# Kernel optimization log

Measured on AMD Instinct MI355X. Metric: run time of the kernel, lower is better.

## Reference

```python
import jax, jax.numpy as jnp
import numpy as np

N_NODES = 50000
N_EDGES = 800000
IN_DIM = 256
HID = [256, 128]
NEG_SLOPE = 0.01  # F.leaky_relu default


def setup_inputs() -> dict:
    key = jax.random.key(0)
    ks = jax.random.split(key, 8)
    x = jax.random.normal(ks[0], (N_NODES, IN_DIM), dtype=jnp.float32)
    w1 = jax.random.normal(ks[1], (IN_DIM, HID[0]), dtype=jnp.float32) * (1.0 / np.sqrt(IN_DIM))
    b1 = jnp.zeros((HID[0],), dtype=jnp.float32)
    w2 = jax.random.normal(ks[2], (HID[0], HID[1]), dtype=jnp.float32) * (1.0 / np.sqrt(HID[0]))
    b2 = jnp.zeros((HID[1],), dtype=jnp.float32)
    src = jax.random.randint(ks[3], (N_EDGES,), 0, N_NODES, dtype=jnp.int32)
    dst = jax.random.randint(ks[4], (N_EDGES,), 0, N_NODES, dtype=jnp.int32)
    edge_weight = jax.random.uniform(ks[5], (N_EDGES,), dtype=jnp.float32)
    return {"x": x, "w1": w1, "b1": b1, "w2": w2, "b2": b2,
            "src": src, "dst": dst, "edge_weight": edge_weight}


def _gcn_layer(h, w, b, src, dst, ew, n_nodes):
    # GraphConvolution: support = h @ W ; out = spmm(adj, support) + b
    support = h @ w                              # [N, d_out]
    msg = support[src] * ew[:, None]             # [E, d_out] gather + scale
    agg = jax.ops.segment_sum(msg, dst, num_segments=n_nodes)  # [N, d_out]
    return agg + b


def reference(x, w1, b1, w2, b2, src, dst, edge_weight):
    # layer 1: GCN -> leaky_relu -> dropout(eval: identity)
    h = _gcn_layer(x, w1, b1, src, dst, edge_weight, N_NODES)
    h = jax.nn.leaky_relu(h, NEG_SLOPE)
    # layer 2
    h = _gcn_layer(h, w2, b2, src, dst, edge_weight, N_NODES)
    h = jax.nn.leaky_relu(h, NEG_SLOPE)
    return h
```

## Files before the change

### kernel.cpp

```cpp
#include <hip/hip_runtime.h>

#define NEG_SLOPE 0.01f

constexpr int N_NODES_C = 50000;
constexpr int N_EDGES_C = 800000;
constexpr int M_PAD = 50048;
constexpr int META_CAP = 950016;

typedef short bf16x8 __attribute__((ext_vector_type(8)));
typedef float f32x4 __attribute__((ext_vector_type(4)));

__device__ inline unsigned short f2bf(float f) {
  unsigned int u = __float_as_uint(f);
  u += 0x7FFF + ((u >> 16) & 1);
  return (unsigned short)(u >> 16);
}
__device__ inline float bf2f(unsigned int h16) {
  return __uint_as_float(h16 << 16);
}

constexpr int NB_CONVX = (M_PAD * 8) / 256;
constexpr int NB_W1 = (256 * 256) / 256;
constexpr int NB_W2 = (256 * 128) / 256;
constexpr int NB_HIST = ((N_EDGES_C / 4) + 255) / 256;
constexpr int NB_NONH = NB_CONVX + NB_W1 + NB_W2;
constexpr int NB_PRE = NB_NONH + NB_HIST;
constexpr int NB_IL = 2 * NB_HIST;

__global__ __launch_bounds__(256) void pre_kernel(
    const float* __restrict__ x, const float* __restrict__ w1,
    const float* __restrict__ w2, const int* __restrict__ dst,
    unsigned short* __restrict__ xb, unsigned short* __restrict__ w1T,
    unsigned short* __restrict__ w2T, int* __restrict__ counts) {
  const int bx = blockIdx.x;
  const int tid = threadIdx.x;
  int l = 0, isHist = 0, h = 0;
  if (bx < NB_IL) {
    if (bx & 1) { isHist = 1; h = bx >> 1; }
    else l = bx >> 1;
  } else {
    l = bx - NB_HIST;
  }

  if (isHist) {
    int e = (h * 256 + tid) * 4;
    if (e < N_EDGES_C) {
      int4 d4 = *(const int4*)(dst + e);
      atomicAdd(&counts[d4.x], 1);
      atomicAdd(&counts[d4.y], 1);
      atomicAdd(&counts[d4.z], 1);
      atomicAdd(&counts[d4.w], 1);
    }
  } else if (l < NB_CONVX) {
    int idx = l * 256 + tid;
    int row = idx >> 3;
    int c32 = (idx & 7) * 32;
    uint4 o[4];
    if (row < N_NODES_C) {
      const float4* p = (const float4*)(x + (size_t)row * 256 + c32);
      float4 f[8];
#pragma unroll
      for (int i = 0; i < 8; ++i) f[i] = p[i];
#pragma unroll
      for (int i = 0; i < 4; ++i) {
        o[i].x = f2bf(f[2 * i].x) | ((unsigned)f2bf(f[2 * i].y) << 16);
        o[i].y = f2bf(f[2 * i].z) | ((unsigned)f2bf(f[2 * i].w) << 16);
        o[i].z = f2bf(f[2 * i + 1].x) | ((unsigned)f2bf(f[2 * i + 1].y) << 16);
        o[i].w = f2bf(f[2 * i + 1].z) | ((unsigned)f2bf(f[2 * i + 1].w) << 16);
      }
    } else {
#pragma unroll
      for (int i = 0; i < 4; ++i) o[i] = make_uint4(0, 0, 0, 0);
    }
#pragma unroll
    for (int i = 0; i < 4; ++i)
      *(uint4*)(xb + (size_t)row * 256 + c32 + i * 8) = o[i];
  } else if (l < NB_CONVX + NB_W1) {
    int idx = (l - NB_CONVX) * 256 + tid;
    int n = idx >> 8, k = idx & 255;
    w1T[idx] = f2bf(w1[(size_t)k * 256 + n]);
  } else {
    int idx = (l - NB_CONVX - NB_W1) * 256 + tid;
    int n = idx >> 8, k = idx & 255;
    w2T[idx] = f2bf(w2[(size_t)k * 128 + n]);
  }
}

constexpr int NB_NODE = (N_NODES_C + 255) / 256;
constexpr int NB_SCAT = (M_PAD + 255) / 256;

__global__ __launch_bounds__(256) void hist_kernel(const int* __restrict__ counts,
                                                   int* __restrict__ hist2,
                                                   int* __restrict__ ehist) {
  __shared__ int lh[64], le[64];
  const int t = threadIdx.x;
  if (t < 64) { lh[t] = 0; le[t] = 0; }
  __syncthreads();
  const int i = blockIdx.x * 256 + t;
  if (i < N_NODES_C) {
    int d = counts[i];
    int bin = d < 63 ? d : 63;
    atomicAdd(&lh[bin], 1);
    atomicAdd(&le[bin], (d + 3) & ~3);
  }
  __syncthreads();
  if (t < 64) {
    if (lh[t]) atomicAdd(&hist2[t], lh[t]);
    if (le[t]) atomicAdd(&ehist[t], le[t]);
  }
}

__global__ __launch_bounds__(256) void scatter_kernel(
    const int* __restrict__ counts, const int* __restrict__ hist2,
    const int* __restrict__ ehist, int* __restrict__ gclaim_n,
    int* __restrict__ gclaim_e, int* __restrict__ perm,
    int* __restrict__ nstart, int* __restrict__ ndeg,
    int* __restrict__ cursor, unsigned* __restrict__ s_meta) {
  __shared__ int nbase[64], ebase[64], lh[64], le[64], gn[64], ge[64];
  const int t = threadIdx.x;
  if (t < 64) {
    int hv = hist2[t], ev = ehist[t];
    int xs = hv, xe = ev;
#pragma unroll
    for (int off = 1; off < 64; off <<= 1) {
      int a = __shfl_up(xs, off);
      int b = __shfl_up(xe, off);
      if (t >= off) { xs += a; xe += b; }
    }
    nbase[t] = xs - hv;
    ebase[t] = xe - ev;
    lh[t] = 0;
    le[t] = 0;
  }
  __syncthreads();
  const int idx = blockIdx.x * 256 + t;
  int d = -1, bin = 0, lrank = 0, erank = 0;
  if (idx < N_NODES_C) {
    d = counts[idx];
    bin = d < 63 ? d : 63;
    lrank = atomicAdd(&lh[bin], 1);
    erank = atomicAdd(&le[bin], (d + 3) & ~3);
  } else if (idx < M_PAD) {
    perm[idx] = idx;
    nstart[idx] = 0;
    ndeg[idx] = 0;
  }
  __syncthreads();
  if (t < 64) {
    gn[t] = lh[t] ? nbase[t] + atomicAdd(&gclaim_n[t], lh[t]) : 0;
    ge[t] = le[t] ? ebase[t] + atomicAdd(&gclaim_e[t], le[t]) : 0;
  }
  __syncthreads();
  if (d >= 0) {
    const int grank = gn[bin] + lrank;
    const int estart = ge[bin] + erank;
    perm[grank] = idx;
    nstart[grank] = estart;
    ndeg[grank] = d;
    cursor[idx] = estart;
    const int d4 = (d + 3) & ~3;
    for (int j = d; j < d4; ++j) s_meta[estart + j] = 0;
  }
}


#define GLOAD_LDS16(g, l)                                              \
  __builtin_amdgcn_global_load_lds(                                    \
      (__attribute__((address_space(1))) void*)(g),                    \
      (__attribute__((address_space(3))) void*)(l), 16, 0, 0)

__device__ __forceinline__ void gemm_tile(
    const unsigned short* __restrict__ A,
    const unsigned short* __restrict__ BT,
    unsigned short* __restrict__ C,
    int N, int ldc, int row0, int col0, short* Asm, short* Bsm) {
  constexpr int K = 256;
  const int tid = threadIdx.x;
  const int lane = tid & 63, wave = tid >> 6;
  const int wm = wave & 1, wn = wave >> 1;

  const int ch0 = wave * 2, ch1 = wave * 2 + 1;
  const int o0 = ch0 * 512 + lane * 8;
  const int o1 = ch1 * 512 + lane * 8;
  const int r0 = o0 >> 5, c0 = o0 & 31;
  const int r1 = o1 >> 5, c1 = o1 & 31;

  f32x4 acc[4][4] = {};

  for (int k0 = 0; k0 < K; k0 += 32) {
    GLOAD_LDS16(A + (size_t)(row0 + r0) * K + k0 + c0, &Asm[ch0 * 512]);
    GLOAD_LDS16(A + (size_t)(row0 + r1) * K + k0 + c1, &Asm[ch1 * 512]);
    GLOAD_LDS16(BT + (size_t)(col0 + r0) * K + k0 + c0, &Bsm[ch0 * 512]);
    GLOAD_LDS16(BT + (size_t)(col0 + r1) * K + k0 + c1, &Bsm[ch1 * 512]);
    __builtin_amdgcn_s_waitcnt(0);
    __syncthreads();

    bf16x8 af[4], bf[4];
#pragma unroll
    for (int mt = 0; mt < 4; ++mt)
      af[mt] = *(const bf16x8*)&Asm[(wm * 64 + mt * 16 + (lane & 15)) * 32 + (lane >> 4) * 8];
#pragma unroll
    for (int nt = 0; nt < 4; ++nt)
      bf[nt] = *(const bf16x8*)&Bsm[(wn * 64 + nt * 16 + (lane & 15)) * 32 + (lane >> 4) * 8];
#pragma unroll
    for (int mt = 0; mt < 4; ++mt)
#pragma unroll
      for (int nt = 0; nt < 4; ++nt)
        acc[mt][nt] = __builtin_amdgcn_mfma_f32_16x16x32_bf16(af[mt], bf[nt], acc[mt][nt], 0, 0, 0);
    __syncthreads();
  }

  const int cl = lane & 15, rq = (lane >> 4) * 4;
#pragma unroll
  for (int mt = 0; mt < 4; ++mt) {
    const int rbase = row0 + wm * 64 + mt * 16 + rq;
#pragma unroll
    for (int nt = 0; nt < 4; ++nt) {
      const int col = col0 + wn * 64 + nt * 16 + cl;
#pragma unroll
      for (int i = 0; i < 4; ++i)
        C[(size_t)(rbase + i) * ldc + col] = f2bf(acc[mt][nt][i]);
    }
  }
}

constexpr int NB_GEMM1 = 2 * (M_PAD / 128);
constexpr int NB_FILL = ((N_EDGES_C / 4) + 255) / 256;

__global__ __launch_bounds__(256) void fill_gemm1_kernel(
    const unsigned short* __restrict__ A, const unsigned short* __restrict__ BT,
    unsigned short* __restrict__ C, const int* __restrict__ src,
    const int* __restrict__ dst, const float* __restrict__ ew,
    int* __restrict__ cursor, unsigned* __restrict__ s_meta) {
  __shared__ short Asm[128 * 32];
  __shared__ short Bsm[128 * 32];
  const int b = blockIdx.x;
  if ((b & 1) == 0) {
    const int t = b >> 1;
    gemm_tile(A, BT, C, 256, 256, (t >> 1) * 128, (t & 1) * 128, Asm, Bsm);
  } else {
    const int g = (b >> 1) * 256 + threadIdx.x;
    const int e = g * 4;
    if (e < N_EDGES_C) {
      int4 d4 = *(const int4*)(dst + e);
      int4 s4 = *(const int4*)(src + e);
      float4 w4 = *(const float4*)(ew + e);
      unsigned m0 = (unsigned)s4.x | ((unsigned)f2bf(w4.x) << 16);
      unsigned m1 = (unsigned)s4.y | ((unsigned)f2bf(w4.y) << 16);
      unsigned m2 = (unsigned)s4.z | ((unsigned)f2bf(w4.z) << 16);
      unsigned m3 = (unsigned)s4.w | ((unsigned)f2bf(w4.w) << 16);
      int p0 = atomicAdd(&cursor[d4.x], 1);
      int p1 = atomicAdd(&cursor[d4.y], 1);
      int p2 = atomicAdd(&cursor[d4.z], 1);
      int p3 = atomicAdd(&cursor[d4.w], 1);
      __builtin_nontemporal_store(m0, s_meta + p0);
      __builtin_nontemporal_store(m1, s_meta + p1);
      __builtin_nontemporal_store(m2, s_meta + p2);
      __builtin_nontemporal_store(m3, s_meta + p3);
    }
  }
}

__global__ __launch_bounds__(256) void gemm2_kernel(
    const unsigned short* __restrict__ A, const unsigned short* __restrict__ BT,
    unsigned short* __restrict__ C) {
  __shared__ short Asm[128 * 32];
  __shared__ short Bsm[128 * 32];
  gemm_tile(A, BT, C, 128, 128, blockIdx.x * 128, 0, Asm, Bsm);
}


__device__ __forceinline__ void rfma_256(float* acc, unsigned m,
                                         const unsigned short* __restrict__ tp) {
  uint2 v = *(const uint2*)(tp + (size_t)(m & 0xffffu) * 256);
  float wt = bf2f(m >> 16);
  acc[0] += bf2f(v.x & 0xffffu) * wt;
  acc[1] += bf2f(v.x >> 16) * wt;
  acc[2] += bf2f(v.y & 0xffffu) * wt;
  acc[3] += bf2f(v.y >> 16) * wt;
}

__device__ __forceinline__ void rfma_128(float* acc, unsigned m,
                                         const unsigned short* __restrict__ tp) {
  unsigned v = *(const unsigned*)(tp + (size_t)(m & 0xffffu) * 128);
  float wt = bf2f(m >> 16);
  acc[0] += bf2f(v & 0xffffu) * wt;
  acc[1] += bf2f(v >> 16) * wt;
}

template <int OUT_D, bool OUT_BF16>
__global__ __launch_bounds__(256) void agg_row_kernel(
    const unsigned short* __restrict__ sup,
    const unsigned* __restrict__ s_meta,
    const int* __restrict__ nstart, const int* __restrict__ ndeg,
    const int* __restrict__ perm, const float* __restrict__ bias,
    unsigned short* __restrict__ out_bf, float* __restrict__ out_f, int n_total) {
  constexpr int DPL = OUT_D / 64;
  const int tid = threadIdx.x;
  const int wv = tid >> 6;
  const int lane = tid & 63;
  const int idx = blockIdx.x * 4 + wv;
  if (idx >= n_total) return;
  const int n = perm[idx];
  const bool valid = n < N_NODES_C;
  const unsigned short* tp = sup + lane * DPL;

  float acc[DPL] = {};
  const int s = nstart[idx];
  const int nq = (ndeg[idx] + 3) >> 2;
  const uint4* mp = (const uint4*)(s_meta + s);

#define RFMA(mm)                              \
  do {                                        \
    if (OUT_D == 256) rfma_256(acc, mm, tp);  \
    else rfma_128(acc, mm, tp);               \
  } while (0)

  if (nq > 0) {
    uint4 m0 = mp[0];
    uint4 m1 = (nq > 1) ? mp[1] : make_uint4(0, 0, 0, 0);
    int q = 0;
    for (; q + 2 < nq; q += 2) {
      uint4 p0 = mp[q + 2];
      uint4 p1 = mp[q + 3];
      RFMA(m0.x); RFMA(m0.y); RFMA(m0.z); RFMA(m0.w);
      RFMA(m1.x); RFMA(m1.y); RFMA(m1.z); RFMA(m1.w);
      m0 = p0;
      m1 = p1;
    }
    RFMA(m0.x); RFMA(m0.y); RFMA(m0.z); RFMA(m0.w);
    if (q + 1 < nq) { RFMA(m1.x); RFMA(m1.y); RFMA(m1.z); RFMA(m1.w); }
  }
#undef RFMA

  const int dbase = lane * DPL;
  if (OUT_BF16) {
    unsigned short o[DPL];
#pragma unroll
    for (int j = 0; j < DPL; ++j) {
      if (valid) {
        float v = acc[j] + bias[dbase + j];
        v = v >= 0.f ? v : NEG_SLOPE * v;
        o[j] = f2bf(v);
      } else {
        o[j] = 0;
      }
    }
    uint2 pk;
    pk.x = o[0] | ((unsigned)o[1] << 16);
    pk.y = o[2] | ((unsigned)o[3] << 16);
    *(uint2*)(out_bf + (size_t)n * OUT_D + dbase) = pk;
  } else if (valid) {
    float r[DPL];
#pragma unroll
    for (int j = 0; j < DPL; ++j) {
      float v = acc[j] + bias[dbase + j];
      r[j] = v >= 0.f ? v : NEG_SLOPE * v;
    }
    *(float2*)(out_f + (size_t)n * OUT_D + dbase) = make_float2(r[0], r[1]);
  }
}


extern "C" void kernel_launch(void* const* d_in, const int* in_sizes, int n_in,
                              void* d_out, int out_size, void* d_ws, size_t ws_size,
                              hipStream_t stream) {
  const float* x  = (const float*)d_in[0];
  const float* w1 = (const float*)d_in[1];
  const float* b1 = (const float*)d_in[2];
  const float* w2 = (const float*)d_in[3];
  const float* b2 = (const float*)d_in[4];
  const int*   src = (const int*)d_in[5];
  const int*   dst = (const int*)d_in[6];
  const float* ew  = (const float*)d_in[7];
  float* out = (float*)d_out;

  unsigned short* xb   = (unsigned short*)d_ws;
  unsigned short* a2b  = xb + (size_t)M_PAD * 256;
  unsigned short* sup1 = a2b + (size_t)M_PAD * 256;
  unsigned short* sup2 = sup1 + (size_t)M_PAD * 256;
  unsigned short* w1T  = sup2 + (size_t)M_PAD * 128;
  unsigned short* w2T  = w1T + 256 * 256;
  int* counts  = (int*)(w2T + 128 * 256);
  int* cursor  = counts + N_NODES_C;
  int* perm    = cursor + N_NODES_C;
  int* nstart  = perm + M_PAD;
  int* ndeg    = nstart + M_PAD;
  int* hist2   = ndeg + M_PAD;
  int* ehist   = hist2 + 64;
  int* gclaim_n= ehist + 64;
  int* gclaim_e= gclaim_n + 64;
  unsigned* s_meta = (unsigned*)(gclaim_e + 64);

  hipMemsetAsync(counts, 0, N_NODES_C * sizeof(int), stream);
  hipMemsetAsync(hist2, 0, 256 * sizeof(int), stream);
  pre_kernel<<<NB_PRE, 256, 0, stream>>>(x, w1, w2, dst, xb, w1T, w2T, counts);

  hist_kernel<<<NB_NODE, 256, 0, stream>>>(counts, hist2, ehist);
  scatter_kernel<<<NB_SCAT, 256, 0, stream>>>(counts, hist2, ehist, gclaim_n,
                                              gclaim_e, perm, nstart, ndeg,
                                              cursor, s_meta);

  fill_gemm1_kernel<<<NB_GEMM1 + NB_FILL, 256, 0, stream>>>(
      xb, w1T, sup1, src, dst, ew, cursor, s_meta);

  agg_row_kernel<256, true><<<M_PAD / 4, 256, 0, stream>>>(
      sup1, s_meta, nstart, ndeg, perm, b1, a2b, nullptr, M_PAD);

  gemm2_kernel<<<M_PAD / 128, 256, 0, stream>>>(a2b, w2T, sup2);
  agg_row_kernel<128, false><<<N_NODES_C / 4, 256, 0, stream>>>(
      sup2, s_meta, nstart, ndeg, perm, b2, nullptr, out, N_NODES_C);
}
```

Before: 296.1 us.

## Split wave across edges with 16-byte gathers and shuffle reduction in aggregation

The row-aggregation kernel now gives each lane 8 features loaded as one 16-byte vector. Sub-groups of the wave handle different edges at the same time, and a cross-lane shuffle reduction combines them at the end. This replaces narrow 4- or 8-byte gathers per lane. Separately, the x-to-bf16 conversion in pre_kernel now uses fully coalesced float4 reads, zeroes the padded rows in a dedicated block, and changes how conversion blocks are interleaved with histogram blocks. The cost is extra shuffles and idle lanes during the epilogue. The 128-dim path also reads padded metadata slots in its tail.

```diff
diff --git a/kernel.cpp b/kernel.cpp
--- a/kernel.cpp
+++ b/kernel.cpp
@@ -19,13 +19,14 @@
   return __uint_as_float(h16 << 16);
 }
 
-constexpr int NB_CONVX = (M_PAD * 8) / 256;
+constexpr int NB_CONV4 = (N_NODES_C * 64) / 1024;
+constexpr int NB_Z = 1;
 constexpr int NB_W1 = (256 * 256) / 256;
 constexpr int NB_W2 = (256 * 128) / 256;
 constexpr int NB_HIST = ((N_EDGES_C / 4) + 255) / 256;
-constexpr int NB_NONH = NB_CONVX + NB_W1 + NB_W2;
+constexpr int NB_NONH = NB_CONV4 + NB_Z + NB_W1 + NB_W2;
 constexpr int NB_PRE = NB_NONH + NB_HIST;
-constexpr int NB_IL = 2 * NB_HIST;
+constexpr int HIST_REGION = NB_HIST * 4;
 
 __global__ __launch_bounds__(256) void pre_kernel(
     const float* __restrict__ x, const float* __restrict__ w1,
@@ -34,10 +35,10 @@
     unsigned short* __restrict__ w2T, int* __restrict__ counts) {
   const int bx = blockIdx.x;
   const int tid = threadIdx.x;
-  int l = 0, isHist = 0, h = 0;
-  if (bx < NB_IL) {
-    if (bx & 1) { isHist = 1; h = bx >> 1; }
-    else l = bx >> 1;
+  int l, isHist = 0, h = 0;
+  if (bx < HIST_REGION) {
+    if ((bx & 3) == 3) { isHist = 1; h = bx >> 2; l = 0; }
+    else l = bx - ((bx + 1) >> 2);
   } else {
     l = bx - NB_HIST;
   }
@@ -51,36 +52,29 @@
       atomicAdd(&counts[d4.z], 1);
       atomicAdd(&counts[d4.w], 1);
     }
-  } else if (l < NB_CONVX) {
-    int idx = l * 256 + tid;
-    int row = idx >> 3;
-    int c32 = (idx & 7) * 32;
-    uint4 o[4];
-    if (row < N_NODES_C) {
-      const float4* p = (const float4*)(x + (size_t)row * 256 + c32);
-      float4 f[8];
-#pragma unroll
-      for (int i = 0; i < 8; ++i) f[i] = p[i];
-#pragma unroll
-      for (int i = 0; i < 4; ++i) {
-        o[i].x = f2bf(f[2 * i].x) | ((unsigned)f2bf(f[2 * i].y) << 16);
-        o[i].y = f2bf(f[2 * i].z) | ((unsigned)f2bf(f[2 * i].w) << 16);
-        o[i].z = f2bf(f[2 * i + 1].x) | ((unsigned)f2bf(f[2 * i + 1].y) << 16);
-        o[i].w = f2bf(f[2 * i + 1].z) | ((unsigned)f2bf(f[2 * i + 1].w) << 16);
-      }
-    } else {
-#pragma unroll
-      for (int i = 0; i < 4; ++i) o[i] = make_uint4(0, 0, 0, 0);
-    }
-#pragma unroll
-    for (int i = 0; i < 4; ++i)
-      *(uint4*)(xb + (size_t)row * 256 + c32 + i * 8) = o[i];
-  } else if (l < NB_CONVX + NB_W1) {
-    int idx = (l - NB_CONVX) * 256 + tid;
+  } else if (l < NB_CONV4) {
+    const float4* xv = (const float4*)x;
+#pragma unroll
+    for (int i = 0; i < 4; ++i) {
+      int g = l * 1024 + i * 256 + tid;
+      float4 f = xv[g];
+      uint2 o;
+      o.x = f2bf(f.x) | ((unsigned)f2bf(f.y) << 16);
+      o.y = f2bf(f.z) | ((unsigned)f2bf(f.w) << 16);
+      *(uint2*)(xb + (size_t)g * 4) = o;
+    }
+  } else if (l == NB_CONV4) {
+    unsigned short* base = xb + (size_t)N_NODES_C * 256;
+    uint4 z = make_uint4(0, 0, 0, 0);
+#pragma unroll
+    for (int i = 0; i < 6; ++i)
+      *(uint4*)(base + (size_t)(i * 256 + tid) * 8) = z;
+  } else if (l < NB_CONV4 + NB_Z + NB_W1) {
+    int idx = (l - NB_CONV4 - NB_Z) * 256 + tid;
     int n = idx >> 8, k = idx & 255;
     w1T[idx] = f2bf(w1[(size_t)k * 256 + n]);
   } else {
-    int idx = (l - NB_CONVX - NB_W1) * 256 + tid;
+    int idx = (l - NB_CONV4 - NB_Z - NB_W1) * 256 + tid;
     int n = idx >> 8, k = idx & 255;
     w2T[idx] = f2bf(w2[(size_t)k * 128 + n]);
   }
@@ -270,22 +264,15 @@
 }
 
 
-__device__ __forceinline__ void rfma_256(float* acc, unsigned m,
-                                         const unsigned short* __restrict__ tp) {
-  uint2 v = *(const uint2*)(tp + (size_t)(m & 0xffffu) * 256);
-  float wt = bf2f(m >> 16);
+__device__ __forceinline__ void fma8v(float* acc, uint4 v, float wt) {
   acc[0] += bf2f(v.x & 0xffffu) * wt;
   acc[1] += bf2f(v.x >> 16) * wt;
   acc[2] += bf2f(v.y & 0xffffu) * wt;
   acc[3] += bf2f(v.y >> 16) * wt;
-}
-
-__device__ __forceinline__ void rfma_128(float* acc, unsigned m,
-                                         const unsigned short* __restrict__ tp) {
-  unsigned v = *(const unsigned*)(tp + (size_t)(m & 0xffffu) * 128);
-  float wt = bf2f(m >> 16);
-  acc[0] += bf2f(v & 0xffffu) * wt;
-  acc[1] += bf2f(v >> 16) * wt;
+  acc[4] += bf2f(v.z & 0xffffu) * wt;
+  acc[5] += bf2f(v.z >> 16) * wt;
+  acc[6] += bf2f(v.w & 0xffffu) * wt;
+  acc[7] += bf2f(v.w >> 16) * wt;
 }
 
 template <int OUT_D, bool OUT_BF16>
@@ -295,7 +282,6 @@
     const int* __restrict__ nstart, const int* __restrict__ ndeg,
     const int* __restrict__ perm, const float* __restrict__ bias,
     unsigned short* __restrict__ out_bf, float* __restrict__ out_f, int n_total) {
-  constexpr int DPL = OUT_D / 64;
   const int tid = threadIdx.x;
   const int wv = tid >> 6;
   const int lane = tid & 63;
@@ -303,61 +289,92 @@
   if (idx >= n_total) return;
   const int n = perm[idx];
   const bool valid = n < N_NODES_C;
-  const unsigned short* tp = sup + lane * DPL;
-
-  float acc[DPL] = {};
   const int s = nstart[idx];
-  const int nq = (ndeg[idx] + 3) >> 2;
-  const uint4* mp = (const uint4*)(s_meta + s);
-
-#define RFMA(mm)                              \
-  do {                                        \
-    if (OUT_D == 256) rfma_256(acc, mm, tp);  \
-    else rfma_128(acc, mm, tp);               \
-  } while (0)
-
-  if (nq > 0) {
-    uint4 m0 = mp[0];
-    uint4 m1 = (nq > 1) ? mp[1] : make_uint4(0, 0, 0, 0);
-    int q = 0;
-    for (; q + 2 < nq; q += 2) {
-      uint4 p0 = mp[q + 2];
-      uint4 p1 = mp[q + 3];
-      RFMA(m0.x); RFMA(m0.y); RFMA(m0.z); RFMA(m0.w);
-      RFMA(m1.x); RFMA(m1.y); RFMA(m1.z); RFMA(m1.w);
-      m0 = p0;
-      m1 = p1;
-    }
-    RFMA(m0.x); RFMA(m0.y); RFMA(m0.z); RFMA(m0.w);
-    if (q + 1 < nq) { RFMA(m1.x); RFMA(m1.y); RFMA(m1.z); RFMA(m1.w); }
-  }
-#undef RFMA
-
-  const int dbase = lane * DPL;
-  if (OUT_BF16) {
-    unsigned short o[DPL];
-#pragma unroll
-    for (int j = 0; j < DPL; ++j) {
+  const int ne4 = ((ndeg[idx] + 3) >> 2) << 2;
+
+  float acc[8] = {};
+
+  if (OUT_D == 256) {
+    const int sub = lane >> 5;
+    const int dl = lane & 31;
+    const unsigned short* tp = sup + dl * 8;
+    for (int j = 0; j < ne4; j += 4) {
+      unsigned ma = s_meta[s + j + sub];
+      unsigned mb = s_meta[s + j + 2 + sub];
+      uint4 va = *(const uint4*)(tp + (size_t)(ma & 0xffffu) * 256);
+      uint4 vb = *(const uint4*)(tp + (size_t)(mb & 0xffffu) * 256);
+      fma8v(acc, va, bf2f(ma >> 16));
+      fma8v(acc, vb, bf2f(mb >> 16));
+    }
+#pragma unroll
+    for (int k = 0; k < 8; ++k) acc[k] += __shfl_xor(acc[k], 32);
+    if (sub == 0) {
+      const int dbase = dl * 8;
+      if (OUT_BF16) {
+        unsigned short o[8];
+#pragma unroll
+        for (int k = 0; k < 8; ++k) {
+          if (valid) {
+            float v = acc[k] + bias[dbase + k];
+            v = v >= 0.f ? v : NEG_SLOPE * v;
+            o[k] = f2bf(v);
+          } else {
+            o[k] = 0;
+          }
+        }
+        uint4 pk;
+        pk.x = o[0] | ((unsigned)o[1] << 16);
+        pk.y = o[2] | ((unsigned)o[3] << 16);
+        pk.z = o[4] | ((unsigned)o[5] << 16);
+        pk.w = o[6] | ((unsigned)o[7] << 16);
+        *(uint4*)(out_bf + (size_t)n * OUT_D + dbase) = pk;
+      } else if (valid) {
+        float r[8];
+#pragma unroll
+        for (int k = 0; k < 8; ++k) {
+          float v = acc[k] + bias[dbase + k];
+          r[k] = v >= 0.f ? v : NEG_SLOPE * v;
+        }
+        *(float4*)(out_f + (size_t)n * OUT_D + dbase) = make_float4(r[0], r[1], r[2], r[3]);
+        *(float4*)(out_f + (size_t)n * OUT_D + dbase + 4) = make_float4(r[4], r[5], r[6], r[7]);
+      }
+    }
+  } else {
+    const int sub = lane >> 4;
+    const int dl = lane & 15;
+    const unsigned short* tp = sup + dl * 8;
+    int j = 0;
+    for (; j + 8 <= ne4; j += 8) {
+      unsigned ma = s_meta[s + j + sub];
+      unsigned mb = s_meta[s + j + 4 + sub];
+      uint4 va = *(const uint4*)(tp + (size_t)(ma & 0xffffu) * 128);
+      uint4 vb = *(const uint4*)(tp + (size_t)(mb & 0xffffu) * 128);
+      fma8v(acc, va, bf2f(ma >> 16));
+      fma8v(acc, vb, bf2f(mb >> 16));
+    }
+    if (j < ne4) {
+      unsigned ma = s_meta[s + j + sub];
+      uint4 va = *(const uint4*)(tp + (size_t)(ma & 0xffffu) * 128);
+      fma8v(acc, va, bf2f(ma >> 16));
+    }
+#pragma unroll
+    for (int k = 0; k < 8; ++k) {
+      acc[k] += __shfl_xor(acc[k], 16);
+      acc[k] += __shfl_xor(acc[k], 32);
+    }
+    if (sub == 0 && lane < 16) {
+      const int dbase = dl * 8;
       if (valid) {
-        float v = acc[j] + bias[dbase + j];
-        v = v >= 0.f ? v : NEG_SLOPE * v;
-        o[j] = f2bf(v);
-      } else {
-        o[j] = 0;
+        float r[8];
+#pragma unroll
+        for (int k = 0; k < 8; ++k) {
+          float v = acc[k] + bias[dbase + k];
+          r[k] = v >= 0.f ? v : NEG_SLOPE * v;
+        }
+        *(float4*)(out_f + (size_t)n * OUT_D + dbase) = make_float4(r[0], r[1], r[2], r[3]);
+        *(float4*)(out_f + (size_t)n * OUT_D + dbase + 4) = make_float4(r[4], r[5], r[6], r[7]);
       }
     }
-    uint2 pk;
-    pk.x = o[0] | ((unsigned)o[1] << 16);
-    pk.y = o[2] | ((unsigned)o[3] << 16);
-    *(uint2*)(out_bf + (size_t)n * OUT_D + dbase) = pk;
-  } else if (valid) {
-    float r[DPL];
-#pragma unroll
-    for (int j = 0; j < DPL; ++j) {
-      float v = acc[j] + bias[dbase + j];
-      r[j] = v >= 0.f ? v : NEG_SLOPE * v;
-    }
-    *(float2*)(out_f + (size_t)n * OUT_D + dbase) = make_float2(r[0], r[1]);
   }
 }
 
```

Measured after the change: 306.1 us. 1.03x slower.

## Make degree-bucket scatter deterministic via per-block prefix counts; reshape x conversion

Applied to the files above, without the earlier changes.

The scatter kernel no longer claims bucket slots with global atomics. The histogram kernel now records per-block bucket counts, and each scatter block sums its predecessors' counts and ranks nodes with wave ballots, which gives stable, node-ordered placement and better locality. The pre-kernel's x-to-bf16 conversion is rewritten to use coalesced float4 loads with a 3:1 interleave against the histogram blocks and a separate zero-pad block. Nontemporal stores of edge metadata become plain stores. The serial per-block prefix loops (up to ~196 iterations) and the 64-iteration ballot loop add latency to the scatter kernel.

```diff
diff --git a/kernel.cpp b/kernel.cpp
--- a/kernel.cpp
+++ b/kernel.cpp
@@ -19,13 +19,14 @@
   return __uint_as_float(h16 << 16);
 }
 
-constexpr int NB_CONVX = (M_PAD * 8) / 256;
+constexpr int NB_CONV4 = (N_NODES_C * 64) / 1024;
+constexpr int NB_Z = 1;
 constexpr int NB_W1 = (256 * 256) / 256;
 constexpr int NB_W2 = (256 * 128) / 256;
 constexpr int NB_HIST = ((N_EDGES_C / 4) + 255) / 256;
-constexpr int NB_NONH = NB_CONVX + NB_W1 + NB_W2;
+constexpr int NB_NONH = NB_CONV4 + NB_Z + NB_W1 + NB_W2;
 constexpr int NB_PRE = NB_NONH + NB_HIST;
-constexpr int NB_IL = 2 * NB_HIST;
+constexpr int HIST_REGION = NB_HIST * 4;
 
 __global__ __launch_bounds__(256) void pre_kernel(
     const float* __restrict__ x, const float* __restrict__ w1,
@@ -34,10 +35,10 @@
     unsigned short* __restrict__ w2T, int* __restrict__ counts) {
   const int bx = blockIdx.x;
   const int tid = threadIdx.x;
-  int l = 0, isHist = 0, h = 0;
-  if (bx < NB_IL) {
-    if (bx & 1) { isHist = 1; h = bx >> 1; }
-    else l = bx >> 1;
+  int l, isHist = 0, h = 0;
+  if (bx < HIST_REGION) {
+    if ((bx & 3) == 3) { isHist = 1; h = bx >> 2; l = 0; }
+    else l = bx - ((bx + 1) >> 2);
   } else {
     l = bx - NB_HIST;
   }
@@ -51,36 +52,29 @@
       atomicAdd(&counts[d4.z], 1);
       atomicAdd(&counts[d4.w], 1);
     }
-  } else if (l < NB_CONVX) {
-    int idx = l * 256 + tid;
-    int row = idx >> 3;
-    int c32 = (idx & 7) * 32;
-    uint4 o[4];
-    if (row < N_NODES_C) {
-      const float4* p = (const float4*)(x + (size_t)row * 256 + c32);
-      float4 f[8];
-#pragma unroll
-      for (int i = 0; i < 8; ++i) f[i] = p[i];
-#pragma unroll
-      for (int i = 0; i < 4; ++i) {
-        o[i].x = f2bf(f[2 * i].x) | ((unsigned)f2bf(f[2 * i].y) << 16);
-        o[i].y = f2bf(f[2 * i].z) | ((unsigned)f2bf(f[2 * i].w) << 16);
-        o[i].z = f2bf(f[2 * i + 1].x) | ((unsigned)f2bf(f[2 * i + 1].y) << 16);
-        o[i].w = f2bf(f[2 * i + 1].z) | ((unsigned)f2bf(f[2 * i + 1].w) << 16);
-      }
-    } else {
-#pragma unroll
-      for (int i = 0; i < 4; ++i) o[i] = make_uint4(0, 0, 0, 0);
-    }
-#pragma unroll
-    for (int i = 0; i < 4; ++i)
-      *(uint4*)(xb + (size_t)row * 256 + c32 + i * 8) = o[i];
-  } else if (l < NB_CONVX + NB_W1) {
-    int idx = (l - NB_CONVX) * 256 + tid;
+  } else if (l < NB_CONV4) {
+    const float4* xv = (const float4*)x;
+#pragma unroll
+    for (int i = 0; i < 4; ++i) {
+      int g = l * 1024 + i * 256 + tid;
+      float4 f = xv[g];
+      uint2 o;
+      o.x = f2bf(f.x) | ((unsigned)f2bf(f.y) << 16);
+      o.y = f2bf(f.z) | ((unsigned)f2bf(f.w) << 16);
+      *(uint2*)(xb + (size_t)g * 4) = o;
+    }
+  } else if (l == NB_CONV4) {
+    unsigned short* base = xb + (size_t)N_NODES_C * 256;
+    uint4 z = make_uint4(0, 0, 0, 0);
+#pragma unroll
+    for (int i = 0; i < 6; ++i)
+      *(uint4*)(base + (size_t)(i * 256 + tid) * 8) = z;
+  } else if (l < NB_CONV4 + NB_Z + NB_W1) {
+    int idx = (l - NB_CONV4 - NB_Z) * 256 + tid;
     int n = idx >> 8, k = idx & 255;
     w1T[idx] = f2bf(w1[(size_t)k * 256 + n]);
   } else {
-    int idx = (l - NB_CONVX - NB_W1) * 256 + tid;
+    int idx = (l - NB_CONV4 - NB_Z - NB_W1) * 256 + tid;
     int n = idx >> 8, k = idx & 255;
     w2T[idx] = f2bf(w2[(size_t)k * 128 + n]);
   }
@@ -91,7 +85,9 @@
 
 __global__ __launch_bounds__(256) void hist_kernel(const int* __restrict__ counts,
                                                    int* __restrict__ hist2,
-                                                   int* __restrict__ ehist) {
+                                                   int* __restrict__ ehist,
+                                                   int* __restrict__ blk_cnt,
+                                                   int* __restrict__ blk_e63) {
   __shared__ int lh[64], le[64];
   const int t = threadIdx.x;
   if (t < 64) { lh[t] = 0; le[t] = 0; }
@@ -107,17 +103,22 @@
   if (t < 64) {
     if (lh[t]) atomicAdd(&hist2[t], lh[t]);
     if (le[t]) atomicAdd(&ehist[t], le[t]);
+    blk_cnt[blockIdx.x * 64 + t] = lh[t];
+    if (t == 63) blk_e63[blockIdx.x] = le[63];
   }
 }
 
 __global__ __launch_bounds__(256) void scatter_kernel(
     const int* __restrict__ counts, const int* __restrict__ hist2,
-    const int* __restrict__ ehist, int* __restrict__ gclaim_n,
-    int* __restrict__ gclaim_e, int* __restrict__ perm,
+    const int* __restrict__ ehist, const int* __restrict__ blk_cnt,
+    const int* __restrict__ blk_e63, int* __restrict__ perm,
     int* __restrict__ nstart, int* __restrict__ ndeg,
     int* __restrict__ cursor, unsigned* __restrict__ s_meta) {
-  __shared__ int nbase[64], ebase[64], lh[64], le[64], gn[64], ge[64];
+  __shared__ int nbase[64], ebase[64], boffn[64], wcnt[4][64], we63s[4];
+  __shared__ int boffe63;
   const int t = threadIdx.x;
+  const int wv = t >> 6, lane = t & 63;
+
   if (t < 64) {
     int hv = hist2[t], ev = ehist[t];
     int xs = hv, xe = ev;
@@ -125,40 +126,68 @@
     for (int off = 1; off < 64; off <<= 1) {
       int a = __shfl_up(xs, off);
       int b = __shfl_up(xe, off);
-      if (t >= off) { xs += a; xe += b; }
+      if (lane >= off) { xs += a; xe += b; }
     }
     nbase[t] = xs - hv;
     ebase[t] = xe - ev;
-    lh[t] = 0;
-    le[t] = 0;
-  }
-  __syncthreads();
+    int bn = 0;
+    for (int b = 0; b < (int)blockIdx.x; ++b) bn += blk_cnt[b * 64 + t];
+    boffn[t] = bn;
+  }
+  if (t == 64) {
+    int be = 0;
+    for (int b = 0; b < (int)blockIdx.x; ++b) be += blk_e63[b];
+    boffe63 = be;
+  }
+
   const int idx = blockIdx.x * 256 + t;
-  int d = -1, bin = 0, lrank = 0, erank = 0;
+  int d = -1, bin = 0, d4 = 0;
   if (idx < N_NODES_C) {
     d = counts[idx];
     bin = d < 63 ? d : 63;
-    lrank = atomicAdd(&lh[bin], 1);
-    erank = atomicAdd(&le[bin], (d + 3) & ~3);
+    d4 = (d + 3) & ~3;
   } else if (idx < M_PAD) {
     perm[idx] = idx;
     nstart[idx] = 0;
     ndeg[idx] = 0;
   }
+
+  int rank_w = 0, mycnt = 0;
+  for (int B = 0; B < 64; ++B) {
+    unsigned long long m = __ballot(d >= 0 && bin == B);
+    if (d >= 0 && bin == B)
+      rank_w = __popcll(m & ((1ull << lane) - 1));
+    if (lane == B) mycnt = __popcll(m);
+  }
+  int c63 = (d >= 0 && bin == 63) ? d4 : 0;
+  int sc = c63;
+#pragma unroll
+  for (int off = 1; off < 64; off <<= 1) {
+    int u = __shfl_up(sc, off);
+    if (lane >= off) sc += u;
+  }
+  const int excl63 = sc - c63;
+  const int tot63 = __shfl(sc, 63);
+  wcnt[wv][lane] = mycnt;
+  if (lane == 0) we63s[wv] = tot63;
   __syncthreads();
-  if (t < 64) {
-    gn[t] = lh[t] ? nbase[t] + atomicAdd(&gclaim_n[t], lh[t]) : 0;
-    ge[t] = le[t] ? ebase[t] + atomicAdd(&gclaim_e[t], le[t]) : 0;
-  }
-  __syncthreads();
+
   if (d >= 0) {
-    const int grank = gn[bin] + lrank;
-    const int estart = ge[bin] + erank;
+    int rank_blk = rank_w;
+    int e63off = excl63;
+    for (int w = 0; w < wv; ++w) {
+      rank_blk += wcnt[w][bin];
+      e63off += we63s[w];
+    }
+    const int grank = nbase[bin] + boffn[bin] + rank_blk;
+    const int d4b = (bin + 3) & ~3;
+    const int estart = (bin < 63)
+        ? ebase[bin] + (boffn[bin] + rank_blk) * d4b
+        : ebase[63] + boffe63 + e63off;
     perm[grank] = idx;
     nstart[grank] = estart;
     ndeg[grank] = d;
     cursor[idx] = estart;
-    const int d4 = (d + 3) & ~3;
     for (int j = d; j < d4; ++j) s_meta[estart + j] = 0;
   }
 }
@@ -253,10 +282,10 @@
       int p1 = atomicAdd(&cursor[d4.y], 1);
       int p2 = atomicAdd(&cursor[d4.z], 1);
       int p3 = atomicAdd(&cursor[d4.w], 1);
-      __builtin_nontemporal_store(m0, s_meta + p0);
-      __builtin_nontemporal_store(m1, s_meta + p1);
-      __builtin_nontemporal_store(m2, s_meta + p2);
-      __builtin_nontemporal_store(m3, s_meta + p3);
+      s_meta[p0] = m0;
+      s_meta[p1] = m1;
+      s_meta[p2] = m2;
+      s_meta[p3] = m3;
     }
   }
 }
@@ -388,17 +417,18 @@
   int* ndeg    = nstart + M_PAD;
   int* hist2   = ndeg + M_PAD;
   int* ehist   = hist2 + 64;
-  int* gclaim_n= ehist + 64;
-  int* gclaim_e= gclaim_n + 64;
-  unsigned* s_meta = (unsigned*)(gclaim_e + 64);
+  int* zspare  = ehist + 64;
+  int* blk_cnt = zspare + 128;
+  int* blk_e63 = blk_cnt + NB_NODE * 64;
+  unsigned* s_meta = (unsigned*)(blk_e63 + NB_NODE);
 
   hipMemsetAsync(counts, 0, N_NODES_C * sizeof(int), stream);
   hipMemsetAsync(hist2, 0, 256 * sizeof(int), stream);
   pre_kernel<<<NB_PRE, 256, 0, stream>>>(x, w1, w2, dst, xb, w1T, w2T, counts);
 
-  hist_kernel<<<NB_NODE, 256, 0, stream>>>(counts, hist2, ehist);
-  scatter_kernel<<<NB_SCAT, 256, 0, stream>>>(counts, hist2, ehist, gclaim_n,
-                                              gclaim_e, perm, nstart, ndeg,
+  hist_kernel<<<NB_NODE, 256, 0, stream>>>(counts, hist2, ehist, blk_cnt, blk_e63);
+  scatter_kernel<<<NB_SCAT, 256, 0, stream>>>(counts, hist2, ehist, blk_cnt,
+                                              blk_e63, perm, nstart, ndeg,
                                               cursor, s_meta);
 
   fill_gemm1_kernel<<<NB_GEMM1 + NB_FILL, 256, 0, stream>>>(
```

Measured after the change: 316.0 us. +6.7%, slower.
